# Kernel optimization log

Measured on AMD Instinct MI355X. Metric: run time of the kernel, lower is better.

Reference implementation:

```python
import jax, jax.numpy as jnp
import numpy as np

C = 51  # num_relation


def setup_inputs() -> dict:
    key = jax.random.key(0)
    N_o, N_u, D = 16384, 16384, 1024
    k = jax.random.split(key, 6)
    feat = jax.random.normal(k[0], (N_o + N_u, D), jnp.float32)
    # first N_o rows are labeled (label != 0), remaining N_u rows unlabeled (label == 0)
    label = jnp.concatenate([
        jax.random.randint(k[1], (N_o,), 1, C),
        jnp.zeros((N_u,), jnp.int32),
    ]).astype(jnp.int32)
    W_o = jax.random.normal(k[2], (C, D), jnp.float32) * 0.03
    b_o = jnp.zeros((C,), jnp.float32)
    W = jax.random.normal(k[3], (C, D), jnp.float32) * 0.03
    b = jnp.zeros((C,), jnp.float32)
    cls = jnp.arange(C)
    group_mid_mask = (cls >= 16) & (cls < 36)   # groups[1]
    group_tail_mask = cls >= 36                 # groups[2]
    # runtime torch.randint partner sampling, hoisted to input construction
    idx_m = jax.random.randint(k[4], (2, N_u), 0, N_o)  # 2 mid copies
    idx_t = jax.random.randint(k[5], (3, N_u), 0, N_o)  # 3 tail copies
    return dict(feat=feat, label=label, W_o=W_o, b_o=b_o, W=W, b=b,
                group_mid_mask=group_mid_mask, group_tail_mask=group_tail_mask,
                idx_m=idx_m, idx_t=idx_t)


def reference(feat, label, W_o, b_o, W, b, group_mid_mask, group_tail_mask, idx_m, idx_t):
    n_u = idx_m.shape[1]
    n_o = feat.shape[0] - n_u
    feat_o, feat_u = feat[:n_o], feat[n_o:]
    label_o = label[:n_o]

    # fc_o under no_grad, then softmax / top-1 rank + score
    logits = jax.lax.stop_gradient(feat_u @ W_o.T + b_o)      # [N_u, C]
    p = jax.nn.softmax(logits, axis=1)
    pred = jnp.argmax(p, axis=1)                               # ranks[:,0]
    score = jnp.max(p, axis=1)                                 # score[:,0]

    # group membership + confidence thresholds (heads are unused in the original)
    mid_m = group_mid_mask[pred] & (score > 0.5)
    tail_m = group_tail_mask[pred] & (score > 0.3)

    oh_u = jax.nn.one_hot(pred, C, dtype=feat.dtype)
    oh_o = jax.nn.one_hot(label_o, C, dtype=feat.dtype)

    im = idx_m.reshape(-1)   # [2*N_u]
    it = idx_t.reshape(-1)   # [3*N_u]

    fm = 0.7 * feat_o[im] + 0.3 * jnp.tile(feat_u, (2, 1))
    lm = 0.7 * oh_o[im] + 0.3 * jnp.tile(oh_u, (2, 1))
    ft = 0.7 * feat_o[it] + 0.3 * jnp.tile(feat_u, (3, 1))
    lt = 0.7 * oh_o[it] + 0.3 * jnp.tile(oh_u, (3, 1))

    feat_cat = jnp.concatenate([fm, ft], axis=0)               # [5*N_u, D]
    label_cat = jnp.concatenate([lm, lt], axis=0)              # [5*N_u, C]
    w = jnp.concatenate([jnp.tile(mid_m, 2), jnp.tile(tail_m, 3)]).astype(feat.dtype)

    # soft-label cross entropy on fc(feat_cat); masked mean over selected rows
    logp = jax.nn.log_softmax(feat_cat @ W.T + b, axis=1)
    ce = -(logp * label_cat).sum(axis=1)
    cnt = w.sum()
    return (ce * w).sum() / jnp.maximum(cnt, 1.0)
```

## Files before the change

kernel.cpp:

```cpp
#include <hip/hip_runtime.h>
#include <math.h>

#define DD 1024
#define SN 52
#define NU 16384
#define NO 16384
#define CEBLK 20480

typedef short short8 __attribute__((ext_vector_type(8)));
typedef float f32x4 __attribute__((ext_vector_type(4)));

__device__ __forceinline__ unsigned short f2b(float x) {
    unsigned int u = __float_as_uint(x);
    u += 0x7FFFu + ((u >> 16) & 1u);
    return (unsigned short)(u >> 16);
}

__device__ __forceinline__ short8 cvt8(float4 a, float4 b) {
    short8 r;
    r[0] = (short)f2b(a.x); r[1] = (short)f2b(a.y);
    r[2] = (short)f2b(a.z); r[3] = (short)f2b(a.w);
    r[4] = (short)f2b(b.x); r[5] = (short)f2b(b.y);
    r[6] = (short)f2b(b.z); r[7] = (short)f2b(b.w);
    return r;
}

__global__ __launch_bounds__(256) void convW(const float* __restrict__ W,
                                             const float* __restrict__ W_o,
                                             unsigned short* __restrict__ Wcat) {
    const int n = blockIdx.x;
    const int k = threadIdx.x * 4;
    const float* src = nullptr;
    if (n < 64) { if (n < 51) src = W + (size_t)n * DD; }
    else        { if (n - 64 < 51) src = W_o + (size_t)(n - 64) * DD; }
    float4 v = src ? *(const float4*)(src + k) : make_float4(0.f, 0.f, 0.f, 0.f);
    ushort4 o;
    o.x = f2b(v.x); o.y = f2b(v.y); o.z = f2b(v.z); o.w = f2b(v.w);
    *(ushort4*)(Wcat + (size_t)n * DD + k) = o;
}

template <int NFR>
__device__ __forceinline__ void gemm_wave(const float* __restrict__ feat,
                                          const unsigned short* __restrict__ Wcat,
                                          const float* __restrict__ b_o,
                                          int m0, float* __restrict__ Bmat,
                                          int* __restrict__ flags) {
    const int lane = threadIdx.x & 63;
    const int w = threadIdx.x >> 6;
    const int col16 = lane & 15;
    const int quad = lane >> 4;
    const float* ap = feat + (size_t)(m0 + w * 16 + col16) * DD + quad * 8;
    const unsigned short* bp = Wcat + (size_t)col16 * DD + quad * 8;

    f32x4 acc[NFR];
#pragma unroll
    for (int nf = 0; nf < NFR; ++nf) acc[nf] = (f32x4){0.f, 0.f, 0.f, 0.f};

    float4 a0 = ((const float4*)ap)[0];
    float4 a1 = ((const float4*)ap)[1];
    short8 bf[NFR];
#pragma unroll
    for (int nf = 0; nf < NFR; ++nf)
        bf[nf] = *(const short8*)(bp + (size_t)nf * 16 * DD);

    for (int k0 = 32; k0 <= DD; k0 += 32) {
        float4 na0, na1;
        short8 nbf[NFR];
        if (k0 < DD) {
            na0 = ((const float4*)(ap + k0))[0];
            na1 = ((const float4*)(ap + k0))[1];
#pragma unroll
            for (int nf = 0; nf < NFR; ++nf)
                nbf[nf] = *(const short8*)(bp + (size_t)nf * 16 * DD + k0);
        }
        const short8 af = cvt8(a0, a1);
#pragma unroll
        for (int nf = 0; nf < NFR; ++nf)
            acc[nf] = __builtin_amdgcn_mfma_f32_16x16x32_bf16(af, bf[nf], acc[nf], 0, 0, 0);
        a0 = na0; a1 = na1;
#pragma unroll
        for (int nf = 0; nf < NFR; ++nf) bf[nf] = nbf[nf];
    }

    const int rbase = m0 + w * 16 + quad * 4;
#pragma unroll
    for (int nf = 0; nf < 4; ++nf) {
        const int colL = nf * 16 + col16;
        if (colL < 51) {
#pragma unroll
            for (int r = 0; r < 4; ++r)
                Bmat[(size_t)(rbase + r) * SN + colL] = acc[nf][r];
        }
    }
    if constexpr (NFR == 8) {
        float boc[4];
#pragma unroll
        for (int c = 0; c < 4; ++c) {
            const int col = c * 16 + col16;
            boc[c] = (col < 51) ? b_o[col] : 0.f;
        }
#pragma unroll
        for (int r = 0; r < 4; ++r) {
            float z[4];
            float m = acc[4][r] + boc[0];
            int mi = col16;
            z[0] = m;
#pragma unroll
            for (int c = 1; c < 4; ++c) {
                const int col = c * 16 + col16;
                z[c] = (col < 51) ? acc[4 + c][r] + boc[c] : -INFINITY;
                if (z[c] > m) { m = z[c]; mi = col; }
            }
#pragma unroll
            for (int off = 1; off < 16; off <<= 1) {
                const float om = __shfl_xor(m, off);
                const int oi = __shfl_xor(mi, off);
                if (om > m || (om == m && oi < mi)) { m = om; mi = oi; }
            }
            float e = 0.f;
#pragma unroll
            for (int c = 0; c < 4; ++c)
                if (c * 16 + col16 < 51) e += expf(z[c] - m);
#pragma unroll
            for (int off = 1; off < 16; off <<= 1) e += __shfl_xor(e, off);
            const float score = 1.f / e;
            const int mid = (mi >= 16 && mi < 36 && score > 0.5f) ? 1 : 0;
            const int tail = (mi >= 36 && score > 0.3f) ? 1 : 0;
            if (col16 == 0) flags[rbase + r - NO] = mi | (mid << 8) | (tail << 9);
        }
    }
}

__global__ __launch_bounds__(256) void gemm_mfma(const float* __restrict__ feat,
                                                 const unsigned short* __restrict__ Wcat,
                                                 const float* __restrict__ b_o,
                                                 float* __restrict__ Bmat,
                                                 int* __restrict__ flags) {
    const int m0 = blockIdx.x * 64;
    if (m0 < NO) gemm_wave<4>(feat, Wcat, b_o, m0, Bmat, flags);
    else         gemm_wave<8>(feat, Wcat, b_o, m0, Bmat, flags);
}

__global__ __launch_bounds__(256) void cekernel(const float* __restrict__ B,
                                                const float* __restrict__ bb,
                                                const int* __restrict__ label,
                                                const int* __restrict__ idxm,
                                                const int* __restrict__ idxt,
                                                const int* __restrict__ flags,
                                                double* __restrict__ pnum,
                                                int* __restrict__ pcnt) {
    __shared__ float snum[4];
    __shared__ int scnt[4];
    const int w = threadIdx.x >> 6;
    const int lane = threadIdx.x & 63;
    const int j = blockIdx.x * 4 + w;
    int u, o, active;
    if (j < 2 * NU) {
        u = j & (NU - 1);
        o = idxm[j];
        active = (flags[u] >> 8) & 1;
    } else {
        const int j2 = j - 2 * NU;
        u = j2 & (NU - 1);
        o = idxt[j2];
        active = (flags[u] >> 9) & 1;
    }
    float ce = 0.f;
    if (active) {
        const float* Bo = B + (size_t)o * SN;
        const float* Bu = B + (size_t)(NO + u) * SN;
        float z = -INFINITY;
        if (lane < 51) z = 0.7f * Bo[lane] + 0.3f * Bu[lane] + bb[lane];
        float m = z;
#pragma unroll
        for (int off = 1; off < 64; off <<= 1) m = fmaxf(m, __shfl_xor(m, off));
        float e = (lane < 51) ? expf(z - m) : 0.f;
#pragma unroll
        for (int off = 1; off < 64; off <<= 1) e += __shfl_xor(e, off);
        const float lse = m + logf(e);
        const int lo = label[o];
        const int pu = flags[u] & 255;
        const float zlo = __shfl(z, lo);
        const float zpu = __shfl(z, pu);
        ce = lse - 0.7f * zlo - 0.3f * zpu;
    }
    if (lane == 0) { snum[w] = ce; scnt[w] = active; }
    __syncthreads();
    if (threadIdx.x == 0) {
        pnum[blockIdx.x] = (double)snum[0] + (double)snum[1] +
                           (double)snum[2] + (double)snum[3];
        pcnt[blockIdx.x] = scnt[0] + scnt[1] + scnt[2] + scnt[3];
    }
}

__global__ __launch_bounds__(256) void finalize(const double* __restrict__ pnum,
                                                const int* __restrict__ pcnt,
                                                float* __restrict__ out) {
    __shared__ double sd[4];
    __shared__ int sc[4];
    const int w = threadIdx.x >> 6;
    const int lane = threadIdx.x & 63;
    double s = 0.0;
    int c = 0;
    for (int i = threadIdx.x; i < CEBLK; i += 256) {
        s += pnum[i];
        c += pcnt[i];
    }
#pragma unroll
    for (int off = 1; off < 64; off <<= 1) {
        s += __shfl_xor(s, off);
        c += __shfl_xor(c, off);
    }
    if (lane == 0) { sd[w] = s; sc[w] = c; }
    __syncthreads();
    if (threadIdx.x == 0) {
        const double n = sd[0] + sd[1] + sd[2] + sd[3];
        const int cc = sc[0] + sc[1] + sc[2] + sc[3];
        out[0] = (float)(n / (cc > 1 ? (double)cc : 1.0));
    }
}

extern "C" void kernel_launch(void* const* d_in, const int* in_sizes, int n_in,
                              void* d_out, int out_size, void* d_ws, size_t ws_size,
                              hipStream_t stream) {
    const float* feat = (const float*)d_in[0];
    const int* label = (const int*)d_in[1];
    const float* W_o = (const float*)d_in[2];
    const float* b_o = (const float*)d_in[3];
    const float* W = (const float*)d_in[4];
    const float* b = (const float*)d_in[5];
    const int* idxm = (const int*)d_in[8];
    const int* idxt = (const int*)d_in[9];

    char* ws = (char*)d_ws;
    float* Bmat = (float*)ws;
    double* pnum = (double*)(ws + 6815744);
    int* pcnt = (int*)(ws + 6815744 + 163840);
    int* flags = (int*)(ws + 6815744 + 163840 + 81920);
    unsigned short* Wcat =
        (unsigned short*)(ws + 6815744 + 163840 + 81920 + 65536);

    convW<<<128, 256, 0, stream>>>(W, W_o, Wcat);
    gemm_mfma<<<(NO + NU) / 64, 256, 0, stream>>>(feat, Wcat, b_o, Bmat, flags);
    cekernel<<<CEBLK, 256, 0, stream>>>(Bmat, b, label, idxm, idxt, flags, pnum, pcnt);
    finalize<<<1, 256, 0, stream>>>(pnum, pcnt, (float*)d_out);
}
```

Measured before the change: 274.9 us.

## Stage feat tiles into LDS with double-buffered async loads; batch CE rows per wave

The GEMM now moves 64x64 fp32 tiles of feat into XOR-swizzled shared memory with global_load_lds, double-buffered across K steps, and reads A fragments from LDS. Previously each lane loaded its own strided rows from global memory. This targets better load coalescing and overlap of global latency with MFMA work, at the cost of a block-wide barrier on every K step. The CE kernel now handles four mixup rows per wave, cutting the block count and partial-sum traffic by four.

```diff
diff --git a/kernel.cpp b/kernel.cpp
--- a/kernel.cpp
+++ b/kernel.cpp
@@ -5,7 +5,7 @@
 #define SN 52
 #define NU 16384
 #define NO 16384
-#define CEBLK 20480
+#define CEBLK 5120
 
 typedef short short8 __attribute__((ext_vector_type(8)));
 typedef float f32x4 __attribute__((ext_vector_type(4)));
@@ -39,53 +39,71 @@
     *(ushort4*)(Wcat + (size_t)n * DD + k) = o;
 }
 
+__device__ __forceinline__ void stage_tile(const float* __restrict__ feat,
+                                           float* __restrict__ buf,
+                                           int m0, int k0, int w, int lane) {
+#pragma unroll
+    for (int i = 0; i < 4; ++i) {
+        const int r = (i * 4 + w) * 4 + (lane >> 4);
+        const int p = lane & 15;
+        const int g = p ^ (r & 7);
+        const float* gp = feat + (size_t)(m0 + r) * DD + k0 + g * 4;
+        __builtin_amdgcn_global_load_lds(
+            (const __attribute__((address_space(1))) void*)gp,
+            (__attribute__((address_space(3))) void*)(buf + (i * 4 + w) * 256),
+            16, 0, 0);
+    }
+}
+
 template <int NFR>
 __device__ __forceinline__ void gemm_wave(const float* __restrict__ feat,
                                           const unsigned short* __restrict__ Wcat,
                                           const float* __restrict__ b_o,
                                           int m0, float* __restrict__ Bmat,
-                                          int* __restrict__ flags) {
-    const int lane = threadIdx.x & 63;
-    const int w = threadIdx.x >> 6;
-    const int col16 = lane & 15;
+                                          int* __restrict__ flags,
+                                          float* __restrict__ As) {
+    const int tid = threadIdx.x;
+    const int lane = tid & 63;
+    const int w = tid >> 6;
+    const int m = lane & 15;
     const int quad = lane >> 4;
-    const float* ap = feat + (size_t)(m0 + w * 16 + col16) * DD + quad * 8;
-    const unsigned short* bp = Wcat + (size_t)col16 * DD + quad * 8;
+    const int s = m & 7;
+    const unsigned short* bp = Wcat + (size_t)m * DD + quad * 8;
 
     f32x4 acc[NFR];
 #pragma unroll
     for (int nf = 0; nf < NFR; ++nf) acc[nf] = (f32x4){0.f, 0.f, 0.f, 0.f};
 
-    float4 a0 = ((const float4*)ap)[0];
-    float4 a1 = ((const float4*)ap)[1];
-    short8 bf[NFR];
-#pragma unroll
-    for (int nf = 0; nf < NFR; ++nf)
-        bf[nf] = *(const short8*)(bp + (size_t)nf * 16 * DD);
-
-    for (int k0 = 32; k0 <= DD; k0 += 32) {
-        float4 na0, na1;
-        short8 nbf[NFR];
-        if (k0 < DD) {
-            na0 = ((const float4*)(ap + k0))[0];
-            na1 = ((const float4*)(ap + k0))[1];
+    stage_tile(feat, As, m0, 0, w, lane);
+
+    for (int kt = 0; kt < 16; ++kt) {
+        float* buf = As + (kt & 1) * 4096;
+        __syncthreads();
+        if (kt < 15)
+            stage_tile(feat, As + ((kt + 1) & 1) * 4096, m0, (kt + 1) * 64, w, lane);
+        short8 breg[2][NFR];
+#pragma unroll
+        for (int h = 0; h < 2; ++h)
 #pragma unroll
             for (int nf = 0; nf < NFR; ++nf)
-                nbf[nf] = *(const short8*)(bp + (size_t)nf * 16 * DD + k0);
-        }
-        const short8 af = cvt8(a0, a1);
-#pragma unroll
-        for (int nf = 0; nf < NFR; ++nf)
-            acc[nf] = __builtin_amdgcn_mfma_f32_16x16x32_bf16(af, bf[nf], acc[nf], 0, 0, 0);
-        a0 = na0; a1 = na1;
-#pragma unroll
-        for (int nf = 0; nf < NFR; ++nf) bf[nf] = nbf[nf];
+                breg[h][nf] = *(const short8*)(bp + (size_t)nf * 16 * DD + kt * 64 + h * 32);
+        const float* arow = buf + (w * 16 + m) * 64;
+#pragma unroll
+        for (int h = 0; h < 2; ++h) {
+            const int c0 = h * 8 + 2 * quad;
+            const float4 f0 = *(const float4*)(arow + ((c0) ^ s) * 4);
+            const float4 f1 = *(const float4*)(arow + ((c0 + 1) ^ s) * 4);
+            const short8 af = cvt8(f0, f1);
+#pragma unroll
+            for (int nf = 0; nf < NFR; ++nf)
+                acc[nf] = __builtin_amdgcn_mfma_f32_16x16x32_bf16(af, breg[h][nf], acc[nf], 0, 0, 0);
+        }
     }
 
     const int rbase = m0 + w * 16 + quad * 4;
 #pragma unroll
     for (int nf = 0; nf < 4; ++nf) {
-        const int colL = nf * 16 + col16;
+        const int colL = nf * 16 + m;
         if (colL < 51) {
 #pragma unroll
             for (int r = 0; r < 4; ++r)
@@ -96,37 +114,37 @@
         float boc[4];
 #pragma unroll
         for (int c = 0; c < 4; ++c) {
-            const int col = c * 16 + col16;
+            const int col = c * 16 + m;
             boc[c] = (col < 51) ? b_o[col] : 0.f;
         }
 #pragma unroll
         for (int r = 0; r < 4; ++r) {
             float z[4];
-            float m = acc[4][r] + boc[0];
-            int mi = col16;
-            z[0] = m;
+            float mx = acc[4][r] + boc[0];
+            int mi = m;
+            z[0] = mx;
 #pragma unroll
             for (int c = 1; c < 4; ++c) {
-                const int col = c * 16 + col16;
+                const int col = c * 16 + m;
                 z[c] = (col < 51) ? acc[4 + c][r] + boc[c] : -INFINITY;
-                if (z[c] > m) { m = z[c]; mi = col; }
+                if (z[c] > mx) { mx = z[c]; mi = col; }
             }
 #pragma unroll
             for (int off = 1; off < 16; off <<= 1) {
-                const float om = __shfl_xor(m, off);
+                const float om = __shfl_xor(mx, off);
                 const int oi = __shfl_xor(mi, off);
-                if (om > m || (om == m && oi < mi)) { m = om; mi = oi; }
+                if (om > mx || (om == mx && oi < mi)) { mx = om; mi = oi; }
             }
             float e = 0.f;
 #pragma unroll
             for (int c = 0; c < 4; ++c)
-                if (c * 16 + col16 < 51) e += expf(z[c] - m);
+                if (c * 16 + m < 51) e += expf(z[c] - mx);
 #pragma unroll
             for (int off = 1; off < 16; off <<= 1) e += __shfl_xor(e, off);
             const float score = 1.f / e;
             const int mid = (mi >= 16 && mi < 36 && score > 0.5f) ? 1 : 0;
             const int tail = (mi >= 36 && score > 0.3f) ? 1 : 0;
-            if (col16 == 0) flags[rbase + r - NO] = mi | (mid << 8) | (tail << 9);
+            if (m == 0) flags[rbase + r - NO] = mi | (mid << 8) | (tail << 9);
         }
     }
 }
@@ -136,9 +154,10 @@
                                                  const float* __restrict__ b_o,
                                                  float* __restrict__ Bmat,
                                                  int* __restrict__ flags) {
+    __shared__ float As[2 * 64 * 64];
     const int m0 = blockIdx.x * 64;
-    if (m0 < NO) gemm_wave<4>(feat, Wcat, b_o, m0, Bmat, flags);
-    else         gemm_wave<8>(feat, Wcat, b_o, m0, Bmat, flags);
+    if (m0 < NO) gemm_wave<4>(feat, Wcat, b_o, m0, Bmat, flags, As);
+    else         gemm_wave<8>(feat, Wcat, b_o, m0, Bmat, flags, As);
 }
 
 __global__ __launch_bounds__(256) void cekernel(const float* __restrict__ B,
@@ -153,38 +172,43 @@
     __shared__ int scnt[4];
     const int w = threadIdx.x >> 6;
     const int lane = threadIdx.x & 63;
-    const int j = blockIdx.x * 4 + w;
-    int u, o, active;
-    if (j < 2 * NU) {
-        u = j & (NU - 1);
-        o = idxm[j];
-        active = (flags[u] >> 8) & 1;
-    } else {
-        const int j2 = j - 2 * NU;
-        u = j2 & (NU - 1);
-        o = idxt[j2];
-        active = (flags[u] >> 9) & 1;
-    }
-    float ce = 0.f;
-    if (active) {
-        const float* Bo = B + (size_t)o * SN;
-        const float* Bu = B + (size_t)(NO + u) * SN;
-        float z = -INFINITY;
-        if (lane < 51) z = 0.7f * Bo[lane] + 0.3f * Bu[lane] + bb[lane];
-        float m = z;
-#pragma unroll
-        for (int off = 1; off < 64; off <<= 1) m = fmaxf(m, __shfl_xor(m, off));
-        float e = (lane < 51) ? expf(z - m) : 0.f;
-#pragma unroll
-        for (int off = 1; off < 64; off <<= 1) e += __shfl_xor(e, off);
-        const float lse = m + logf(e);
-        const int lo = label[o];
-        const int pu = flags[u] & 255;
-        const float zlo = __shfl(z, lo);
-        const float zpu = __shfl(z, pu);
-        ce = lse - 0.7f * zlo - 0.3f * zpu;
-    }
-    if (lane == 0) { snum[w] = ce; scnt[w] = active; }
+    float csum = 0.f;
+    int ccnt = 0;
+#pragma unroll
+    for (int it = 0; it < 4; ++it) {
+        const int j = (blockIdx.x * 4 + w) * 4 + it;
+        int u, o, active;
+        if (j < 2 * NU) {
+            u = j & (NU - 1);
+            o = idxm[j];
+            active = (flags[u] >> 8) & 1;
+        } else {
+            const int j2 = j - 2 * NU;
+            u = j2 & (NU - 1);
+            o = idxt[j2];
+            active = (flags[u] >> 9) & 1;
+        }
+        if (active) {
+            const float* Bo = B + (size_t)o * SN;
+            const float* Bu = B + (size_t)(NO + u) * SN;
+            float z = -INFINITY;
+            if (lane < 51) z = 0.7f * Bo[lane] + 0.3f * Bu[lane] + bb[lane];
+            float m = z;
+#pragma unroll
+            for (int off = 1; off < 64; off <<= 1) m = fmaxf(m, __shfl_xor(m, off));
+            float e = (lane < 51) ? expf(z - m) : 0.f;
+#pragma unroll
+            for (int off = 1; off < 64; off <<= 1) e += __shfl_xor(e, off);
+            const float lse = m + logf(e);
+            const int lo = label[o];
+            const int pu = flags[u] & 255;
+            const float zlo = __shfl(z, lo);
+            const float zpu = __shfl(z, pu);
+            csum += lse - 0.7f * zlo - 0.3f * zpu;
+            ccnt += 1;
+        }
+    }
+    if (lane == 0) { snum[w] = csum; scnt[w] = ccnt; }
     __syncthreads();
     if (threadIdx.x == 0) {
         pnum[blockIdx.x] = (double)snum[0] + (double)snum[1] +
@@ -235,10 +259,10 @@
     char* ws = (char*)d_ws;
     float* Bmat = (float*)ws;
     double* pnum = (double*)(ws + 6815744);
-    int* pcnt = (int*)(ws + 6815744 + 163840);
-    int* flags = (int*)(ws + 6815744 + 163840 + 81920);
+    int* pcnt = (int*)(ws + 6815744 + 40960);
+    int* flags = (int*)(ws + 6815744 + 40960 + 20480);
     unsigned short* Wcat =
-        (unsigned short*)(ws + 6815744 + 163840 + 81920 + 65536);
+        (unsigned short*)(ws + 6815744 + 40960 + 20480 + 65536);
 
     convW<<<128, 256, 0, stream>>>(W, W_o, Wcat);
     gemm_mfma<<<(NO + NU) / 64, 256, 0, stream>>>(feat, Wcat, b_o, Bmat, flags);
```

After: 241.7 us. 1.14x faster.
